# Performance work log

Measured on AMD Instinct MI355X. Metric: run time of the kernel, lower is better.

## Reference

```python
import jax, jax.numpy as jnp
import numpy as np

B, T, D, H = 4, 2048, 1024, 16
HD = D // H
EPS = 1e-5


def gelu_tanh(x):
    c = jnp.sqrt(jnp.asarray(2.0 / jnp.pi, x.dtype))
    return 0.5 * x * (1.0 + jnp.tanh(c * (x + 0.044715 * x * x * x)))


def layernorm(x, gamma, beta):
    mean = jnp.mean(x, axis=-1, keepdims=True)
    var = jnp.var(x, axis=-1, keepdims=True)
    return gamma * (x - mean) / jnp.sqrt(var + EPS) + beta


def setup_inputs() -> dict:
    key = jax.random.key(0)
    ks = jax.random.split(key, 12)
    s = 0.02
    return {
        "x": jax.random.normal(ks[0], (B, T, D), jnp.float32),
        "Wq": jax.random.normal(ks[1], (D, D), jnp.float32) * s,
        "Wk": jax.random.normal(ks[2], (D, D), jnp.float32) * s,
        "Wv": jax.random.normal(ks[3], (D, D), jnp.float32) * s,
        "Wo": jax.random.normal(ks[4], (D, D), jnp.float32) * s,
        "bo": jnp.zeros((D,), jnp.float32),
        "W1": jax.random.normal(ks[5], (D, 4 * D), jnp.float32) * s,
        "b1": jnp.zeros((4 * D,), jnp.float32),
        "W2": jax.random.normal(ks[6], (4 * D, D), jnp.float32) * s,
        "b2": jnp.zeros((D,), jnp.float32),
        "gamma1": jnp.ones((D,), jnp.float32),
        "beta1": jnp.zeros((D,), jnp.float32),
        "gamma2": jnp.ones((D,), jnp.float32),
        "beta2": jnp.zeros((D,), jnp.float32),
    }


def reference(x, Wq, Wk, Wv, Wo, bo, W1, b1, W2, b2, gamma1, beta1, gamma2, beta2):
    # --- attention sublayer (pre-norm, causal) ---
    h = layernorm(x, gamma1, beta1)
    q = (h @ Wq).reshape(B, T, H, HD).transpose(0, 2, 1, 3)  # (B,H,T,hd)
    k = (h @ Wk).reshape(B, T, H, HD).transpose(0, 2, 1, 3)
    v = (h @ Wv).reshape(B, T, H, HD).transpose(0, 2, 1, 3)
    scores = jnp.einsum("bhqd,bhkd->bhqk", q, k) * (HD ** -0.5)
    causal = jnp.tril(jnp.ones((T, T), bool))
    scores = jnp.where(causal, scores, -jnp.inf)
    w = jax.nn.softmax(scores, axis=-1)
    attn = jnp.einsum("bhqk,bhkd->bhqd", w, v).transpose(0, 2, 1, 3).reshape(B, T, D)
    x = x + (attn @ Wo + bo)
    # --- FFN sublayer ---
    h2 = layernorm(x, gamma2, beta2)
    ff = gelu_tanh(h2 @ W1 + b1) @ W2 + b2
    return x + ff
```

## Files before the change

### kernel.cpp

```cpp
#include <hip/hip_runtime.h>
#include <hip/hip_bf16.h>


typedef __bf16 bf16;
typedef __attribute__((ext_vector_type(8))) __bf16 bf16x8;
typedef __attribute__((ext_vector_type(4))) __bf16 bf16x4;
typedef __attribute__((ext_vector_type(4))) float floatx4;

#define EXPC 0.18033688011112042f

__device__ __forceinline__ void async_cp16(const bf16* g, bf16* l) {
  __builtin_amdgcn_global_load_lds(
      (const __attribute__((address_space(1))) void*)g,
      (__attribute__((address_space(3))) void*)l, 16, 0, 0);
}

__global__ __launch_bounds__(256) void transpose_cvt(
    const float* __restrict__ W, bf16* __restrict__ WT, int K, int N) {
  __shared__ bf16 tile[32][33];
  const int tn = blockIdx.x;
  const int tk = blockIdx.y;
  const int t = threadIdx.x;
  const int row = t >> 3;
  const int c4 = (t & 7) * 4;

  const float* src = W + (size_t)(tk * 32 + row) * N + tn * 32 + c4;
  float4 v = *(const float4*)src;
  tile[row][c4 + 0] = (bf16)v.x;
  tile[row][c4 + 1] = (bf16)v.y;
  tile[row][c4 + 2] = (bf16)v.z;
  tile[row][c4 + 3] = (bf16)v.w;
  __syncthreads();
  bf16x4 o;
  o[0] = tile[c4 + 0][row];
  o[1] = tile[c4 + 1][row];
  o[2] = tile[c4 + 2][row];
  o[3] = tile[c4 + 3][row];
  *(bf16x4*)(WT + (size_t)(tn * 32 + row) * K + tk * 32 + c4) = o;
}

__global__ __launch_bounds__(256) void ln_kernel(
    const float* __restrict__ x, const float* __restrict__ gamma,
    const float* __restrict__ beta, bf16* __restrict__ out) {
  const int row = blockIdx.x;
  const int t = threadIdx.x;
  const float* xr = x + (size_t)row * 1024;
  float4 v4 = *(const float4*)(xr + t * 4);
  float a[4] = {v4.x, v4.y, v4.z, v4.w};
  float s = a[0] + a[1] + a[2] + a[3];
  float ss = a[0] * a[0] + a[1] * a[1] + a[2] * a[2] + a[3] * a[3];
  for (int off = 1; off < 64; off <<= 1) {
    s += __shfl_xor(s, off);
    ss += __shfl_xor(ss, off);
  }
  __shared__ float red[8];
  const int wid = t >> 6, lane = t & 63;
  if (lane == 0) { red[wid] = s; red[wid + 4] = ss; }
  __syncthreads();
  s = red[0] + red[1] + red[2] + red[3];
  ss = red[4] + red[5] + red[6] + red[7];
  const float mean = s * (1.0f / 1024.0f);
  const float var = ss * (1.0f / 1024.0f) - mean * mean;
  const float rstd = rsqrtf(var + 1e-5f);
  bf16x4 o;
  for (int j = 0; j < 4; ++j) {
    float g = gamma[t * 4 + j];
    float b = beta[t * 4 + j];
    o[j] = (bf16)((a[j] - mean) * rstd * g + b);
  }
  *(bf16x4*)(out + (size_t)row * 1024 + t * 4) = o;
}

__device__ __forceinline__ float gelu_f(float x) {
  const float c = 0.7978845608028654f;
  float u = c * (x + 0.044715f * x * x * x);
  return 0.5f * x * (1.0f + tanhf(u));
}

template <int MODE>
__global__ __launch_bounds__(256, 2) void gemm_bt(
    const bf16* __restrict__ A, const bf16* __restrict__ BT,
    const float* __restrict__ bias, const float* __restrict__ resid,
    void* __restrict__ out, int M, int N, int K) {
  __shared__ bf16 sA[128 * 32];
  __shared__ bf16 sB[128 * 32];
  const int t = threadIdx.x;
  const int lane = t & 63, wid = t >> 6;
  const int waveM = wid >> 1, waveN = wid & 1;
  const int quad = lane >> 4, l16 = lane & 15;
  const size_t m0 = (size_t)blockIdx.x * 128;
  const size_t n0 = (size_t)blockIdx.y * 128;

  floatx4 acc[4][4] = {};

  const int srow = wid * 16 + (lane >> 2);
  const int scol = (lane & 3) * 8;
  const bf16* Ag = A + (m0 + srow) * (size_t)K + scol;
  const bf16* Bg = BT + (n0 + srow) * (size_t)K + scol;
  bf16* sAp = sA + wid * 512 + lane * 8;
  bf16* sBp = sB + wid * 512 + lane * 8;

  for (int k0 = 0; k0 < K; k0 += 32) {
    __syncthreads();
    async_cp16(Ag + k0, sAp);
    async_cp16(Ag + (size_t)64 * K + k0, sAp + 64 * 32);
    async_cp16(Bg + k0, sBp);
    async_cp16(Bg + (size_t)64 * K + k0, sBp + 64 * 32);
    __syncthreads();
    bf16x8 af[4], bfv[4];
#pragma unroll
    for (int i = 0; i < 4; ++i)
      af[i] = *(const bf16x8*)&sA[(waveM * 64 + i * 16 + l16) * 32 + quad * 8];
#pragma unroll
    for (int i = 0; i < 4; ++i)
      bfv[i] = *(const bf16x8*)&sB[(waveN * 64 + i * 16 + l16) * 32 + quad * 8];
#pragma unroll
    for (int mt = 0; mt < 4; ++mt)
#pragma unroll
      for (int nt = 0; nt < 4; ++nt)
        acc[mt][nt] = __builtin_amdgcn_mfma_f32_16x16x32_bf16(
            af[mt], bfv[nt], acc[mt][nt], 0, 0, 0);
  }

#pragma unroll
  for (int mt = 0; mt < 4; ++mt) {
#pragma unroll
    for (int nt = 0; nt < 4; ++nt) {
      const size_t row_base = m0 + waveM * 64 + mt * 16 + quad * 4;
      const size_t col = n0 + waveN * 64 + nt * 16 + l16;
#pragma unroll
      for (int r = 0; r < 4; ++r) {
        const size_t row = row_base + r;
        float v = acc[mt][nt][r];
        if (MODE == 1) {
          v = gelu_f(v + bias[col]);
          ((bf16*)out)[row * N + col] = (bf16)v;
        } else if (MODE == 2) {
          v += bias[col] + resid[row * N + col];
          ((float*)out)[row * N + col] = v;
        } else {
          ((bf16*)out)[row * N + col] = (bf16)v;
        }
      }
    }
  }
}

__global__ __launch_bounds__(256) void attn_kernel(
    const bf16* __restrict__ QKV, bf16* __restrict__ O) {
  const int idx = blockIdx.x;
  const int qt = 31 - (idx >> 6);
  const int bh = idx & 63;
  const int b = bh >> 4, h = bh & 15;
  const int t = threadIdx.x;
  const int lane = t & 63, wid = t >> 6;
  const int quad = lane >> 4, l16 = lane & 15;

  __shared__ bf16 sQ[64][72];
  __shared__ bf16 sK[64][72];
  __shared__ bf16 sVt[64][72];
  __shared__ bf16 sP[4][16][72];

  const size_t qbase = (size_t)b * 2048 * 3072 + (size_t)h * 64;
  const size_t kbase = qbase + 1024;
  const size_t vbase = qbase + 2048;
  const int q0 = qt * 64;

  for (int c = t; c < 512; c += 256) {
    int row = c >> 3, sub = (c & 7) * 8;
    *(bf16x8*)&sQ[row][sub] =
        *(const bf16x8*)(QKV + qbase + (size_t)(q0 + row) * 3072 + sub);
  }
  __syncthreads();

  bf16x8 aq[2];
  aq[0] = *(const bf16x8*)&sQ[wid * 16 + l16][quad * 8];
  aq[1] = *(const bf16x8*)&sQ[wid * 16 + l16][32 + quad * 8];

  float l_part[4] = {0.f, 0.f, 0.f, 0.f};
  floatx4 o_acc[4] = {};

  for (int kt = 0; kt <= qt; ++kt) {
    __syncthreads();
    const int k0 = kt * 64;
    for (int c = t; c < 512; c += 256) {
      int row = c >> 3, sub = (c & 7) * 8;
      *(bf16x8*)&sK[row][sub] =
          *(const bf16x8*)(QKV + kbase + (size_t)(k0 + row) * 3072 + sub);
      bf16x8 v8 = *(const bf16x8*)(QKV + vbase + (size_t)(k0 + row) * 3072 + sub);
#pragma unroll
      for (int j = 0; j < 8; ++j)
        sVt[sub + j][row ^ (sub & 56)] = v8[j];
    }
    __syncthreads();

    float p[4][4];
#pragma unroll
    for (int nt = 0; nt < 4; ++nt) {
      floatx4 acc = {};
#pragma unroll
      for (int ks = 0; ks < 2; ++ks) {
        bf16x8 bk = *(const bf16x8*)&sK[nt * 16 + l16][ks * 32 + quad * 8];
        acc = __builtin_amdgcn_mfma_f32_16x16x32_bf16(aq[ks], bk, acc, 0, 0, 0);
      }
#pragma unroll
      for (int r = 0; r < 4; ++r) p[nt][r] = exp2f(acc[r] * EXPC);
    }

    if (kt == qt) {
      const int qrow_base = q0 + wid * 16 + quad * 4;
#pragma unroll
      for (int nt = 0; nt < 4; ++nt) {
        const int kk = k0 + nt * 16 + l16;
#pragma unroll
        for (int r = 0; r < 4; ++r)
          if (kk > qrow_base + r) p[nt][r] = 0.f;
      }
    }

#pragma unroll
    for (int nt = 0; nt < 4; ++nt)
#pragma unroll
      for (int r = 0; r < 4; ++r) {
        l_part[r] += p[nt][r];
        sP[wid][quad * 4 + r][nt * 16 + l16] = (bf16)p[nt][r];
      }

    bf16x8 ap[2];
    ap[0] = *(const bf16x8*)&sP[wid][l16][quad * 8];
    ap[1] = *(const bf16x8*)&sP[wid][l16][32 + quad * 8];
#pragma unroll
    for (int nt = 0; nt < 4; ++nt) {
      const int r2 = nt * 16 + l16;
#pragma unroll
      for (int ks = 0; ks < 2; ++ks) {
        bf16x8 bv =
            *(const bf16x8*)&sVt[r2][(ks * 32 + quad * 8) ^ (r2 & 56)];
        o_acc[nt] =
            __builtin_amdgcn_mfma_f32_16x16x32_bf16(ap[ks], bv, o_acc[nt], 0, 0, 0);
      }
    }
  }

#pragma unroll
  for (int off = 1; off < 16; off <<= 1)
#pragma unroll
    for (int r = 0; r < 4; ++r) l_part[r] += __shfl_xor(l_part[r], off);
  float inv[4];
#pragma unroll
  for (int r = 0; r < 4; ++r) inv[r] = 1.0f / l_part[r];

#pragma unroll
  for (int nt = 0; nt < 4; ++nt)
#pragma unroll
    for (int r = 0; r < 4; ++r) {
      const size_t row = (size_t)b * 2048 + q0 + wid * 16 + quad * 4 + r;
      const size_t col = (size_t)h * 64 + nt * 16 + l16;
      O[row * 1024 + col] = (bf16)(o_acc[nt][r] * inv[r]);
    }
}

extern "C" void kernel_launch(void* const* d_in, const int* in_sizes, int n_in,
                              void* d_out, int out_size, void* d_ws, size_t ws_size,
                              hipStream_t stream) {
  const float* x = (const float*)d_in[0];
  const float* Wq = (const float*)d_in[1];
  const float* Wk = (const float*)d_in[2];
  const float* Wv = (const float*)d_in[3];
  const float* Wo = (const float*)d_in[4];
  const float* bo = (const float*)d_in[5];
  const float* W1 = (const float*)d_in[6];
  const float* b1 = (const float*)d_in[7];
  const float* W2 = (const float*)d_in[8];
  const float* b2 = (const float*)d_in[9];
  const float* gamma1 = (const float*)d_in[10];
  const float* beta1 = (const float*)d_in[11];
  const float* gamma2 = (const float*)d_in[12];
  const float* beta2 = (const float*)d_in[13];

  char* ws = (char*)d_ws;
  const size_t MB = (size_t)1 << 20;
  bf16* WqkvT = (bf16*)(ws + 0 * MB);
  bf16* WoT = (bf16*)(ws + 6 * MB);
  bf16* W1T = (bf16*)(ws + 8 * MB);
  bf16* W2T = (bf16*)(ws + 16 * MB);
  bf16* h1  = (bf16*)(ws + 24 * MB);
  bf16* QKVb = (bf16*)(ws + 40 * MB);
  bf16* attnb = (bf16*)(ws + 88 * MB);
  float* x1 = (float*)(ws + 104 * MB);
  bf16* h2  = (bf16*)(ws + 136 * MB);
  bf16* midb = (bf16*)(ws + 152 * MB);

  dim3 blk(256);

  transpose_cvt<<<dim3(32, 32), blk, 0, stream>>>(Wq, WqkvT, 1024, 1024);
  transpose_cvt<<<dim3(32, 32), blk, 0, stream>>>(Wk, WqkvT + (size_t)1024 * 1024, 1024, 1024);
  transpose_cvt<<<dim3(32, 32), blk, 0, stream>>>(Wv, WqkvT + (size_t)2048 * 1024, 1024, 1024);
  transpose_cvt<<<dim3(32, 32), blk, 0, stream>>>(Wo, WoT, 1024, 1024);
  transpose_cvt<<<dim3(128, 32), blk, 0, stream>>>(W1, W1T, 1024, 4096);
  transpose_cvt<<<dim3(32, 128), blk, 0, stream>>>(W2, W2T, 4096, 1024);

  ln_kernel<<<8192, blk, 0, stream>>>(x, gamma1, beta1, h1);

  gemm_bt<3><<<dim3(64, 24), blk, 0, stream>>>(h1, WqkvT, nullptr, nullptr,
                                               QKVb, 8192, 3072, 1024);

  attn_kernel<<<dim3(2048), blk, 0, stream>>>(QKVb, attnb);

  gemm_bt<2><<<dim3(64, 8), blk, 0, stream>>>(attnb, WoT, bo, x, x1, 8192, 1024, 1024);

  ln_kernel<<<8192, blk, 0, stream>>>(x1, gamma2, beta2, h2);

  gemm_bt<1><<<dim3(64, 32), blk, 0, stream>>>(h2, W1T, b1, nullptr, midb, 8192, 4096, 1024);

  gemm_bt<2><<<dim3(64, 8), blk, 0, stream>>>(midb, W2T, b2, x1, d_out, 8192, 1024, 4096);
}
```

Measured before the change: 528.6 us.

## Use 512-thread GEMM for N=1024 projections and batch small weight transposes

Adds a 512-thread (8-wave) variant of the bf16 MFMA GEMM with the same 128x128 tile, where each wave computes a 64x32 subtile. It is used for the Wo and W2 projections, which launch only 512 blocks, so more waves run per CU and latency is better hidden. The four 1024x1024 weight transposes are also merged into one launch with a z-dimension to save launch overhead. Per-wave MFMA work per LDS load drops, which may reduce compute efficiency.

```diff
diff --git a/kernel.cpp b/kernel.cpp
--- a/kernel.cpp
+++ b/kernel.cpp
@@ -13,6 +13,37 @@
   __builtin_amdgcn_global_load_lds(
       (const __attribute__((address_space(1))) void*)g,
       (__attribute__((address_space(3))) void*)l, 16, 0, 0);
+}
+
+__global__ __launch_bounds__(256) void transpose_cvt4(
+    const float* __restrict__ S0, const float* __restrict__ S1,
+    const float* __restrict__ S2, const float* __restrict__ S3,
+    bf16* __restrict__ D0, bf16* __restrict__ D1, bf16* __restrict__ D2,
+    bf16* __restrict__ D3, int K, int N) {
+  const float* W = (blockIdx.z == 0) ? S0 : (blockIdx.z == 1) ? S1
+                   : (blockIdx.z == 2) ? S2 : S3;
+  bf16* WT = (blockIdx.z == 0) ? D0 : (blockIdx.z == 1) ? D1
+             : (blockIdx.z == 2) ? D2 : D3;
+  __shared__ bf16 tile[32][33];
+  const int tn = blockIdx.x;
+  const int tk = blockIdx.y;
+  const int t = threadIdx.x;
+  const int row = t >> 3;
+  const int c4 = (t & 7) * 4;
+
+  const float* src = W + (size_t)(tk * 32 + row) * N + tn * 32 + c4;
+  float4 v = *(const float4*)src;
+  tile[row][c4 + 0] = (bf16)v.x;
+  tile[row][c4 + 1] = (bf16)v.y;
+  tile[row][c4 + 2] = (bf16)v.z;
+  tile[row][c4 + 3] = (bf16)v.w;
+  __syncthreads();
+  bf16x4 o;
+  o[0] = tile[c4 + 0][row];
+  o[1] = tile[c4 + 1][row];
+  o[2] = tile[c4 + 2][row];
+  o[3] = tile[c4 + 3][row];
+  *(bf16x4*)(WT + (size_t)(tn * 32 + row) * K + tk * 32 + c4) = o;
 }
 
 __global__ __launch_bounds__(256) void transpose_cvt(
@@ -128,6 +159,73 @@
     for (int nt = 0; nt < 4; ++nt) {
       const size_t row_base = m0 + waveM * 64 + mt * 16 + quad * 4;
       const size_t col = n0 + waveN * 64 + nt * 16 + l16;
+#pragma unroll
+      for (int r = 0; r < 4; ++r) {
+        const size_t row = row_base + r;
+        float v = acc[mt][nt][r];
+        if (MODE == 1) {
+          v = gelu_f(v + bias[col]);
+          ((bf16*)out)[row * N + col] = (bf16)v;
+        } else if (MODE == 2) {
+          v += bias[col] + resid[row * N + col];
+          ((float*)out)[row * N + col] = v;
+        } else {
+          ((bf16*)out)[row * N + col] = (bf16)v;
+        }
+      }
+    }
+  }
+}
+
+template <int MODE>
+__global__ __launch_bounds__(512, 4) void gemm_bt8(
+    const bf16* __restrict__ A, const bf16* __restrict__ BT,
+    const float* __restrict__ bias, const float* __restrict__ resid,
+    void* __restrict__ out, int M, int N, int K) {
+  __shared__ bf16 sA[128 * 32];
+  __shared__ bf16 sB[128 * 32];
+  const int t = threadIdx.x;
+  const int lane = t & 63, wid = t >> 6;
+  const int waveM = wid >> 2, waveN = wid & 3;
+  const int quad = lane >> 4, l16 = lane & 15;
+  const size_t m0 = (size_t)blockIdx.x * 128;
+  const size_t n0 = (size_t)blockIdx.y * 128;
+
+  floatx4 acc[4][2] = {};
+
+  const int srow = wid * 16 + (lane >> 2);
+  const int scol = (lane & 3) * 8;
+  const bf16* Ag = A + (m0 + srow) * (size_t)K + scol;
+  const bf16* Bg = BT + (n0 + srow) * (size_t)K + scol;
+  bf16* sAp = sA + wid * 512 + lane * 8;
+  bf16* sBp = sB + wid * 512 + lane * 8;
+
+  for (int k0 = 0; k0 < K; k0 += 32) {
+    __syncthreads();
+    async_cp16(Ag + k0, sAp);
+    async_cp16(Bg + k0, sBp);
+    __syncthreads();
+    bf16x8 af[4], bfv[2];
+#pragma unroll
+    for (int i = 0; i < 4; ++i)
+      af[i] = *(const bf16x8*)&sA[(waveM * 64 + i * 16 + l16) * 32 + quad * 8];
+#pragma unroll
+    for (int i = 0; i < 2; ++i)
+      bfv[i] = *(const bf16x8*)&sB[(waveN * 32 + i * 16 + l16) * 32 + quad * 8];
+#pragma unroll
+    for (int mt = 0; mt < 4; ++mt)
+#pragma unroll
+      for (int nt = 0; nt < 2; ++nt)
+        acc[mt][nt] = __builtin_amdgcn_mfma_f32_16x16x32_bf16(
+            af[mt], bfv[nt], acc[mt][nt], 0, 0, 0);
+  }
+
+#pragma unroll
+  for (int mt = 0; mt < 4; ++mt) {
+#pragma unroll
+    for (int nt = 0; nt < 2; ++nt) {
+      const size_t row_base = m0 + waveM * 64 + mt * 16 + quad * 4;
+      const size_t col = n0 + waveN * 32 + nt * 16 + l16;
 #pragma unroll
       for (int r = 0; r < 4; ++r) {
         const size_t row = row_base + r;
@@ -293,10 +391,9 @@
 
   dim3 blk(256);
 
-  transpose_cvt<<<dim3(32, 32), blk, 0, stream>>>(Wq, WqkvT, 1024, 1024);
-  transpose_cvt<<<dim3(32, 32), blk, 0, stream>>>(Wk, WqkvT + (size_t)1024 * 1024, 1024, 1024);
-  transpose_cvt<<<dim3(32, 32), blk, 0, stream>>>(Wv, WqkvT + (size_t)2048 * 1024, 1024, 1024);
-  transpose_cvt<<<dim3(32, 32), blk, 0, stream>>>(Wo, WoT, 1024, 1024);
+  transpose_cvt4<<<dim3(32, 32, 4), blk, 0, stream>>>(
+      Wq, Wk, Wv, Wo, WqkvT, WqkvT + (size_t)1024 * 1024,
+      WqkvT + (size_t)2048 * 1024, WoT, 1024, 1024);
   transpose_cvt<<<dim3(128, 32), blk, 0, stream>>>(W1, W1T, 1024, 4096);
   transpose_cvt<<<dim3(32, 128), blk, 0, stream>>>(W2, W2T, 4096, 1024);
 
@@ -307,11 +404,14 @@
 
   attn_kernel<<<dim3(2048), blk, 0, stream>>>(QKVb, attnb);
 
-  gemm_bt<2><<<dim3(64, 8), blk, 0, stream>>>(attnb, WoT, bo, x, x1, 8192, 1024, 1024);
+  gemm_bt8<2><<<dim3(64, 8), dim3(512), 0, stream>>>(attnb, WoT, bo, x, x1,
+                                                     8192, 1024, 1024);
 
   ln_kernel<<<8192, blk, 0, stream>>>(x1, gamma2, beta2, h2);
 
-  gemm_bt<1><<<dim3(64, 32), blk, 0, stream>>>(h2, W1T, b1, nullptr, midb, 8192, 4096, 1024);
-
-  gemm_bt<2><<<dim3(64, 8), blk, 0, stream>>>(midb, W2T, b2, x1, d_out, 8192, 1024, 4096);
-}
+  gemm_bt<1><<<dim3(64, 32), blk, 0, stream>>>(h2, W1T, b1, nullptr, midb,
+                                               8192, 4096, 1024);
+
+  gemm_bt8<2><<<dim3(64, 8), dim3(512), 0, stream>>>(midb, W2T, b2, x1, d_out,
+                                                     8192, 1024, 4096);
+}
```

New measurement: 539.3 us. 2.0% more time.

## Split-K the W2 GEMM with atomic accumulation and batch small weight transposes

Applied to the files above, without the earlier changes.

The final FFN down-projection GEMM (K=4096, only 512 blocks) is split into two K halves via a z-grid dimension, with partial results atomically added into an output pre-initialised by a new kernel holding residual plus bias. This aims to raise occupancy and parallelism for the long-K GEMM, at the cost of an extra pass over the output and fp32 atomic traffic. The four 1024x1024 weight transposes are merged into one launch using blockIdx.z to cut launch overhead.

```diff
diff --git a/kernel.cpp b/kernel.cpp
--- a/kernel.cpp
+++ b/kernel.cpp
@@ -13,6 +13,37 @@
   __builtin_amdgcn_global_load_lds(
       (const __attribute__((address_space(1))) void*)g,
       (__attribute__((address_space(3))) void*)l, 16, 0, 0);
+}
+
+__global__ __launch_bounds__(256) void transpose_cvt4(
+    const float* __restrict__ S0, const float* __restrict__ S1,
+    const float* __restrict__ S2, const float* __restrict__ S3,
+    bf16* __restrict__ D0, bf16* __restrict__ D1, bf16* __restrict__ D2,
+    bf16* __restrict__ D3, int K, int N) {
+  const float* W = (blockIdx.z == 0) ? S0 : (blockIdx.z == 1) ? S1
+                   : (blockIdx.z == 2) ? S2 : S3;
+  bf16* WT = (blockIdx.z == 0) ? D0 : (blockIdx.z == 1) ? D1
+             : (blockIdx.z == 2) ? D2 : D3;
+  __shared__ bf16 tile[32][33];
+  const int tn = blockIdx.x;
+  const int tk = blockIdx.y;
+  const int t = threadIdx.x;
+  const int row = t >> 3;
+  const int c4 = (t & 7) * 4;
+
+  const float* src = W + (size_t)(tk * 32 + row) * N + tn * 32 + c4;
+  float4 v = *(const float4*)src;
+  tile[row][c4 + 0] = (bf16)v.x;
+  tile[row][c4 + 1] = (bf16)v.y;
+  tile[row][c4 + 2] = (bf16)v.z;
+  tile[row][c4 + 3] = (bf16)v.w;
+  __syncthreads();
+  bf16x4 o;
+  o[0] = tile[c4 + 0][row];
+  o[1] = tile[c4 + 1][row];
+  o[2] = tile[c4 + 2][row];
+  o[3] = tile[c4 + 3][row];
+  *(bf16x4*)(WT + (size_t)(tn * 32 + row) * K + tk * 32 + c4) = o;
 }
 
 __global__ __launch_bounds__(256) void transpose_cvt(
@@ -71,6 +102,17 @@
   *(bf16x4*)(out + (size_t)row * 1024 + t * 4) = o;
 }
 
+__global__ __launch_bounds__(256) void init_resid_bias(
+    const float* __restrict__ resid, const float* __restrict__ bias,
+    float* __restrict__ out) {
+  const size_t row = blockIdx.x;
+  const int t = threadIdx.x;
+  float4 r = *(const float4*)(resid + row * 1024 + t * 4);
+  float4 b = *(const float4*)(bias + t * 4);
+  r.x += b.x; r.y += b.y; r.z += b.z; r.w += b.w;
+  *(float4*)(out + row * 1024 + t * 4) = r;
+}
+
 __device__ __forceinline__ float gelu_f(float x) {
   const float c = 0.7978845608028654f;
   float u = c * (x + 0.044715f * x * x * x);
@@ -81,7 +123,7 @@
 __global__ __launch_bounds__(256, 2) void gemm_bt(
     const bf16* __restrict__ A, const bf16* __restrict__ BT,
     const float* __restrict__ bias, const float* __restrict__ resid,
-    void* __restrict__ out, int M, int N, int K) {
+    void* __restrict__ out, int M, int N, int K, int kChunk) {
   __shared__ bf16 sA[128 * 32];
   __shared__ bf16 sB[128 * 32];
   const int t = threadIdx.x;
@@ -90,6 +132,8 @@
   const int quad = lane >> 4, l16 = lane & 15;
   const size_t m0 = (size_t)blockIdx.x * 128;
   const size_t n0 = (size_t)blockIdx.y * 128;
+  const int kBegin = blockIdx.z * kChunk;
+  const int kEnd = kBegin + kChunk;
 
   floatx4 acc[4][4] = {};
 
@@ -100,7 +144,7 @@
   bf16* sAp = sA + wid * 512 + lane * 8;
   bf16* sBp = sB + wid * 512 + lane * 8;
 
-  for (int k0 = 0; k0 < K; k0 += 32) {
+  for (int k0 = kBegin; k0 < kEnd; k0 += 32) {
     __syncthreads();
     async_cp16(Ag + k0, sAp);
     async_cp16(Ag + (size_t)64 * K + k0, sAp + 64 * 32);
@@ -138,6 +182,8 @@
         } else if (MODE == 2) {
           v += bias[col] + resid[row * N + col];
           ((float*)out)[row * N + col] = v;
+        } else if (MODE == 4) {
+          atomicAdd(&((float*)out)[row * N + col], v);
         } else {
           ((bf16*)out)[row * N + col] = (bf16)v;
         }
@@ -293,25 +339,28 @@
 
   dim3 blk(256);
 
-  transpose_cvt<<<dim3(32, 32), blk, 0, stream>>>(Wq, WqkvT, 1024, 1024);
-  transpose_cvt<<<dim3(32, 32), blk, 0, stream>>>(Wk, WqkvT + (size_t)1024 * 1024, 1024, 1024);
-  transpose_cvt<<<dim3(32, 32), blk, 0, stream>>>(Wv, WqkvT + (size_t)2048 * 1024, 1024, 1024);
-  transpose_cvt<<<dim3(32, 32), blk, 0, stream>>>(Wo, WoT, 1024, 1024);
+  transpose_cvt4<<<dim3(32, 32, 4), blk, 0, stream>>>(
+      Wq, Wk, Wv, Wo, WqkvT, WqkvT + (size_t)1024 * 1024,
+      WqkvT + (size_t)2048 * 1024, WoT, 1024, 1024);
   transpose_cvt<<<dim3(128, 32), blk, 0, stream>>>(W1, W1T, 1024, 4096);
   transpose_cvt<<<dim3(32, 128), blk, 0, stream>>>(W2, W2T, 4096, 1024);
 
   ln_kernel<<<8192, blk, 0, stream>>>(x, gamma1, beta1, h1);
 
   gemm_bt<3><<<dim3(64, 24), blk, 0, stream>>>(h1, WqkvT, nullptr, nullptr,
-                                               QKVb, 8192, 3072, 1024);
+                                               QKVb, 8192, 3072, 1024, 1024);
 
   attn_kernel<<<dim3(2048), blk, 0, stream>>>(QKVb, attnb);
 
-  gemm_bt<2><<<dim3(64, 8), blk, 0, stream>>>(attnb, WoT, bo, x, x1, 8192, 1024, 1024);
+  gemm_bt<2><<<dim3(64, 8), blk, 0, stream>>>(attnb, WoT, bo, x, x1,
+                                              8192, 1024, 1024, 1024);
 
   ln_kernel<<<8192, blk, 0, stream>>>(x1, gamma2, beta2, h2);
 
-  gemm_bt<1><<<dim3(64, 32), blk, 0, stream>>>(h2, W1T, b1, nullptr, midb, 8192, 4096, 1024);
-
-  gemm_bt<2><<<dim3(64, 8), blk, 0, stream>>>(midb, W2T, b2, x1, d_out, 8192, 1024, 4096);
-}
+  gemm_bt<1><<<dim3(64, 32), blk, 0, stream>>>(h2, W1T, b1, nullptr, midb,
+                                               8192, 4096, 1024, 1024);
+
+  init_resid_bias<<<8192, blk, 0, stream>>>(x1, b2, (float*)d_out);
+  gemm_bt<4><<<dim3(64, 8, 2), blk, 0, stream>>>(midb, W2T, nullptr, nullptr,
+                                                 d_out, 8192, 1024, 4096, 2048);
+}
```

New measurement: 565.6 us. 7.0% more time.
